# Performance work log

Hardware: AMD Instinct MI355X
Metric: run time of the kernel (lower is better)

## Reference

```python
import jax, jax.numpy as jnp
import numpy as np

D_MODEL = 768
D_FF = 3072
N_BEHAVIORS = 4
EPS = 1e-12


def layer_norm(x, g, b):
    m = jnp.mean(x, axis=-1, keepdims=True)
    v = jnp.mean(jnp.square(x - m), axis=-1, keepdims=True)
    return (x - m) * jax.lax.rsqrt(v + EPS) * g + b


def setup_inputs() -> dict:
    key = jax.random.key(0)
    ks = jax.random.split(key, 8)
    B, L = 8, 2048
    s1 = 1.0 / np.sqrt(D_MODEL)
    s2 = 1.0 / np.sqrt(D_FF)
    return {
        "input_tensor": jax.random.normal(ks[0], (B, L, D_MODEL), dtype=jnp.float32),
        "type_seq": jax.random.randint(ks[1], (B, L), 0, N_BEHAVIORS + 1),
        # per-behavior FeedForward params, stacked on leading n dim
        "W1": jax.random.normal(ks[2], (N_BEHAVIORS, D_MODEL, D_FF), dtype=jnp.float32) * s1,
        "b1": jnp.zeros((N_BEHAVIORS, D_FF), dtype=jnp.float32),
        "W2": jax.random.normal(ks[3], (N_BEHAVIORS, D_FF, D_MODEL), dtype=jnp.float32) * s2,
        "b2": jnp.zeros((N_BEHAVIORS, D_MODEL), dtype=jnp.float32),
        "ln_g": jnp.ones((N_BEHAVIORS, D_MODEL), dtype=jnp.float32),
        "ln_b": jnp.zeros((N_BEHAVIORS, D_MODEL), dtype=jnp.float32),
        # outer LayerNorm params
        "out_g": jnp.ones((D_MODEL,), dtype=jnp.float32),
        "out_b": jnp.zeros((D_MODEL,), dtype=jnp.float32),
    }


def reference(input_tensor, type_seq, W1, b1, W2, b2, ln_g, ln_b, out_g, out_b):
    n = W1.shape[0]
    # run every behavior's FeedForward over the full sequence (dense over-compute)
    h = jnp.einsum('BLH,nHF->nBLF', input_tensor, W1) + b1[:, None, None, :]
    h = jax.nn.gelu(h, approximate=False)  # torch 'gelu' = exact erf form
    h = jnp.einsum('nBLF,nFH->nBLH', h, W2) + b2[:, None, None, :]
    # per-expert residual LayerNorm (FeedForward with residual=True)
    h = layer_norm(h + input_tensor[None], ln_g[:, None, None, :], ln_b[:, None, None, :])
    # prepend zeros branch (class 0 = padding) then one-hot select per token
    stacked = jnp.concatenate([jnp.zeros_like(input_tensor)[None], h], axis=0)  # [n+1,B,L,H]
    onehot = jax.nn.one_hot(type_seq, n + 1, dtype=input_tensor.dtype)  # [B,L,n+1]
    sel = jnp.einsum('nBLH,BLn->BLH', stacked, onehot)
    # dropout is identity in eval; fused residual + LayerNorm
    return layer_norm(sel + input_tensor, out_g, out_b)
```

## Files before the change

kernel.cpp:

```cpp
#include <hip/hip_runtime.h>
#include <hip/hip_bf16.h>
#include <math.h>

#define NTOK   16384
#define DM     768
#define DF     3072
#define NEXP   4
#define TILE_SH (128 * 32)

#define XBLKS  6144
#define W1BLKS 2304
#define W2BLKS 2304
#define PREP_BLKS (1 + XBLKS + W1BLKS + W2BLKS)

typedef short bf16x8 __attribute__((ext_vector_type(8)));
typedef float f32x4  __attribute__((ext_vector_type(4)));

#define WS_CNT    0u
#define WS_BASES  256u
#define WS_POS    512u
#define WS_LIST   (512u + 65536u)
#define WS_XB     (WS_LIST + 262144u)
#define WS_W1T    (WS_XB + 25165824u)
#define WS_W2T    (WS_W1T + 18874368u)
#define WS_H1     (WS_W2T + 18874368u)
#define WS_H2     (WS_H1 + 100663296u)
#define WS_END    (WS_H2 + 25165824u)

__device__ __forceinline__ ushort f2bf(float f) {
    unsigned int v; __builtin_memcpy(&v, &f, 4);
    v = v + 0x7fffu + ((v >> 16) & 1u);
    return (ushort)(v >> 16);
}
__device__ __forceinline__ float bf2f(ushort u) {
    unsigned int v = ((unsigned int)u) << 16;
    float f; __builtin_memcpy(&f, &v, 4); return f;
}

__device__ __forceinline__ float fast_gelu(float v) {
    float y = v + 0.044715f * v * v * v;
    float e = __builtin_amdgcn_exp2f(-2.3022082f * y);
    return v * __builtin_amdgcn_rcpf(1.0f + e);
}

typedef __attribute__((address_space(1))) const void gvoid_t;
typedef __attribute__((address_space(3))) void lvoid_t;
__device__ __forceinline__ void cp16(const void* g, void* l) {
    __builtin_amdgcn_global_load_lds((gvoid_t*)g, (lvoid_t*)l, 16, 0, 0);
}

__device__ __forceinline__ int xcd_remap(int id, int T) {
    const int q = T >> 3, r = T & 7;
    const int x = id & 7, j = id >> 3;
    return (x < r ? x * (q + 1) : r * (q + 1) + (x - r) * q) + j;
}

__device__ __forceinline__ void transpose_tile(
    const float* __restrict__ src, ushort* __restrict__ dst, int R, int C,
    int bx, int by, int tid, ushort* tile ) {
    const int r0 = by * 64, c0 = bx * 64;
#pragma unroll
    for (int q = 0; q < 2; ++q) {
        int li = q * 256 + tid;
        int r = li >> 3, c = (li & 7) * 8;
        const float* s = src + (size_t)(r0 + r) * C + (c0 + c);
        float4 v0 = *(const float4*)s;
        float4 v1 = *(const float4*)(s + 4);
        ushort tmp[8];
        tmp[0] = f2bf(v0.x); tmp[1] = f2bf(v0.y); tmp[2] = f2bf(v0.z); tmp[3] = f2bf(v0.w);
        tmp[4] = f2bf(v1.x); tmp[5] = f2bf(v1.y); tmp[6] = f2bf(v1.z); tmp[7] = f2bf(v1.w);
        int sw = (((c >> 3) ^ ((r >> 3) & 7)) << 3);
        *(uint4*)&tile[r * 72 + sw] = *(uint4*)tmp;
    }
    __syncthreads();
#pragma unroll
    for (int q = 0; q < 2; ++q) {
        int li = q * 256 + tid;
        int r = li >> 3, c = (li & 7) * 8;
        ushort tmp[8];
#pragma unroll
        for (int j = 0; j < 8; ++j)
            tmp[j] = tile[(c + j) * 72 +
                          ((((r >> 3) & 7) ^ (((c + j) >> 3) & 7)) << 3) + (r & 7)];
        *(uint4*)(dst + (size_t)(c0 + r) * R + (r0 + c)) = *(uint4*)tmp;
    }
}

__global__ __launch_bounds__(256) void prep_kernel(
    const int* __restrict__ type_seq, const float* __restrict__ X,
    const float* __restrict__ W1, const float* __restrict__ W2,
    int* __restrict__ cnt, int* __restrict__ bases,
    int* __restrict__ pos_of, int* __restrict__ list,
    ushort* __restrict__ Xb, ushort* __restrict__ W1t, ushort* __restrict__ W2t) {
    __shared__ ushort tile[64 * 72];
    __shared__ int lcnt[NEXP];
    const int tid = threadIdx.x;
    const int bid = blockIdx.x;

    if (bid == 0) {
        if (tid < NEXP) lcnt[tid] = 0;
        __syncthreads();
        const int lane = tid & 63;
        for (int it = 0; it < NTOK / 256; ++it) {
            int t = it * 256 + tid;
            int k = type_seq[t];
#pragma unroll
            for (int e = 0; e < NEXP; ++e) {
                unsigned long long m = __ballot(k == e + 1);
                int total = __popcll(m);
                int b = 0;
                if (lane == 0 && total) b = atomicAdd(&lcnt[e], total);
                b = __shfl(b, 0, 64);
                if (k == e + 1) {
                    int p = b + __popcll(m & ((1ull << lane) - 1ull));
                    list[e * NTOK + p] = t;
                    pos_of[t] = p;
                }
            }
        }
        __syncthreads();
        if (tid == 0) {
            int s = 0, mb = 0;
            for (int e = 0; e < NEXP; ++e) {
                cnt[e] = lcnt[e];
                bases[e] = s;
                bases[8 + e] = mb;
                s += lcnt[e];
                mb += (lcnt[e] + 127) >> 7;
            }
            bases[12] = mb;
        }
        return;
    }

    int id = bid - 1;
    if (id < XBLKS) {
        size_t i = (size_t)(id * 256 + tid) * 8;
        float4 v0 = *(const float4*)(X + i);
        float4 v1 = *(const float4*)(X + i + 4);
        ushort tmp[8];
        tmp[0] = f2bf(v0.x); tmp[1] = f2bf(v0.y); tmp[2] = f2bf(v0.z); tmp[3] = f2bf(v0.w);
        tmp[4] = f2bf(v1.x); tmp[5] = f2bf(v1.y); tmp[6] = f2bf(v1.z); tmp[7] = f2bf(v1.w);
        *(uint4*)(Xb + i) = *(uint4*)tmp;
        return;
    }
    id -= XBLKS;
    if (id < W1BLKS) {
        int z = id / 576, r = id % 576;
        size_t mb = (size_t)z * DM * DF;
        transpose_tile(W1 + mb, W1t + mb, DM, DF, r % 48, r / 48, tid, tile);
        return;
    }
    id -= W1BLKS;
    {
        int z = id / 576, r = id % 576;
        size_t mb = (size_t)z * DF * DM;
        transpose_tile(W2 + mb, W2t + mb, DF, DM, r % 12, r / 12, tid, tile);
    }
}


__global__ __launch_bounds__(512, 4) void gemm1_kernel(
    const ushort* __restrict__ Xb, const ushort* __restrict__ W1t,
    const float* __restrict__ b1, const int* __restrict__ cnt,
    const int* __restrict__ bases, const int* __restrict__ list,
    ushort* __restrict__ h1) {
    const int mb = bases[12];
    const int T = mb * 24;
    int id = blockIdx.y * 24 + blockIdx.x;
    if (id >= T) return;
    id = xcd_remap(id, T);
    const int y = id / 24;
    const int n0 = (id % 24) * 128;
    const int* mboff = bases + 8;
    const int e = (y >= mboff[1]) + (y >= mboff[2]) + (y >= mboff[3]);
    const int m0 = (y - mboff[e]) << 7;
    const int count = cnt[e];
    const int NK = DM / 32;

    __shared__ __align__(16) short As[2 * TILE_SH];
    __shared__ __align__(16) short Bs[2 * TILE_SH];

    const int tid = threadIdx.x;
    const int wave = tid >> 6, lane = tid & 63;
    const int wm = (wave & 1) * 64, wn = (wave >> 1) * 32;
    const int lrow = lane & 15;
    const int qg = lane >> 4;

    int r0 = min(m0 + (tid >> 2), count - 1);
    int t0 = list[e * NTOK + r0];
    const int qsrc = ((tid & 3) ^ ((tid >> 3) & 3)) * 8;
    const ushort* a0 = Xb + (size_t)t0 * DM + qsrc;
    const ushort* Wb = W1t + (size_t)e * DF * DM;
    const ushort* bp0 = Wb + (size_t)(n0 + (tid >> 2)) * DM + qsrc;

    short* aDst = As + tid * 8;
    short* bDst = Bs + tid * 8;

    int aOff[4], bOff[2];
#pragma unroll
    for (int i = 0; i < 4; ++i) {
        int ra = wm + i * 16 + lrow;
        aOff[i] = ra * 32 + (qg ^ ((ra >> 1) & 3)) * 8;
    }
#pragma unroll
    for (int j = 0; j < 2; ++j) {
        int rb = wn + j * 16 + lrow;
        bOff[j] = rb * 32 + (qg ^ ((rb >> 1) & 3)) * 8;
    }

    f32x4 z = {0.f, 0.f, 0.f, 0.f};
    f32x4 acc[4][2];
#pragma unroll
    for (int i = 0; i < 4; ++i)
#pragma unroll
        for (int j = 0; j < 2; ++j) acc[i][j] = z;

    cp16(a0, aDst); cp16(bp0, bDst);
    a0 += 32; bp0 += 32;

    for (int ks = 0; ks < NK; ++ks) {
        __syncthreads();
        const int nsel = ((ks + 1) & 1) * TILE_SH;
        if (ks + 1 < NK) {
            cp16(a0, aDst + nsel); cp16(bp0, bDst + nsel);
            a0 += 32; bp0 += 32;
        }
        const short* Ab = As + (ks & 1) * TILE_SH;
        const short* Bb = Bs + (ks & 1) * TILE_SH;
        bf16x8 av[4], bv[2];
#pragma unroll
        for (int i = 0; i < 4; ++i) av[i] = *(const bf16x8*)(Ab + aOff[i]);
#pragma unroll
        for (int j = 0; j < 2; ++j) bv[j] = *(const bf16x8*)(Bb + bOff[j]);
#pragma unroll
        for (int i = 0; i < 4; ++i)
#pragma unroll
            for (int j = 0; j < 2; ++j)
                acc[i][j] = __builtin_amdgcn_mfma_f32_16x16x32_bf16(av[i], bv[j], acc[i][j], 0, 0, 0);
    }

    const int base = bases[e];
    float bias[2];
#pragma unroll
    for (int nt = 0; nt < 2; ++nt)
        bias[nt] = b1[e * DF + n0 + wn + nt * 16 + lrow];
#pragma unroll
    for (int mt = 0; mt < 4; ++mt) {
        int gm = m0 + wm + mt * 16 + (lane >> 4) * 4;
#pragma unroll
        for (int nt = 0; nt < 2; ++nt) {
            int gn = n0 + wn + nt * 16 + lrow;
#pragma unroll
            for (int r = 0; r < 4; ++r) {
                int i = gm + r;
                if (i < count) {
                    float v = acc[mt][nt][r] + bias[nt];
                    h1[(size_t)(base + i) * DF + gn] = f2bf(fast_gelu(v));
                }
            }
        }
    }
}

__global__ __launch_bounds__(512, 4) void gemm2_kernel(
    const ushort* __restrict__ h1, const ushort* __restrict__ W2t,
    const float* __restrict__ b2, const int* __restrict__ cnt,
    const int* __restrict__ bases, ushort* __restrict__ h2) {
    const int mb = bases[12];
    const int T = mb * 6;
    int id = blockIdx.y * 6 + blockIdx.x;
    if (id >= T) return;
    id = xcd_remap(id, T);
    const int y = id / 6;
    const int n0 = (id % 6) * 128;
    const int* mboff = bases + 8;
    const int e = (y >= mboff[1]) + (y >= mboff[2]) + (y >= mboff[3]);
    const int m0 = (y - mboff[e]) << 7;
    const int count = cnt[e];
    const int base = bases[e];
    const int NK = DF / 32;

    __shared__ __align__(16) short As[2 * TILE_SH];
    __shared__ __align__(16) short Bs[2 * TILE_SH];

    const int tid = threadIdx.x;
    const int wave = tid >> 6, lane = tid & 63;
    const int wm = (wave & 1) * 64, wn = (wave >> 1) * 32;
    const int lrow = lane & 15;
    const int qg = lane >> 4;

    int r0 = min(m0 + (tid >> 2), count - 1);
    const int qsrc = ((tid & 3) ^ ((tid >> 3) & 3)) * 8;
    const ushort* a0 = h1 + (size_t)(base + r0) * DF + qsrc;
    const ushort* Wb = W2t + (size_t)e * DM * DF;
    const ushort* bp0 = Wb + (size_t)(n0 + (tid >> 2)) * DF + qsrc;

    short* aDst = As + tid * 8;
    short* bDst = Bs + tid * 8;

    int aOff[4], bOff[2];
#pragma unroll
    for (int i = 0; i < 4; ++i) {
        int ra = wm + i * 16 + lrow;
        aOff[i] = ra * 32 + (qg ^ ((ra >> 1) & 3)) * 8;
    }
#pragma unroll
    for (int j = 0; j < 2; ++j) {
        int rb = wn + j * 16 + lrow;
        bOff[j] = rb * 32 + (qg ^ ((rb >> 1) & 3)) * 8;
    }

    f32x4 z = {0.f, 0.f, 0.f, 0.f};
    f32x4 acc[4][2];
#pragma unroll
    for (int i = 0; i < 4; ++i)
#pragma unroll
        for (int j = 0; j < 2; ++j) acc[i][j] = z;

    cp16(a0, aDst); cp16(bp0, bDst);
    a0 += 32; bp0 += 32;

    for (int ks = 0; ks < NK; ++ks) {
        __syncthreads();
        const int nsel = ((ks + 1) & 1) * TILE_SH;
        if (ks + 1 < NK) {
            cp16(a0, aDst + nsel); cp16(bp0, bDst + nsel);
            a0 += 32; bp0 += 32;
        }
        const short* Ab = As + (ks & 1) * TILE_SH;
        const short* Bb = Bs + (ks & 1) * TILE_SH;
        bf16x8 av[4], bv[2];
#pragma unroll
        for (int i = 0; i < 4; ++i) av[i] = *(const bf16x8*)(Ab + aOff[i]);
#pragma unroll
        for (int j = 0; j < 2; ++j) bv[j] = *(const bf16x8*)(Bb + bOff[j]);
#pragma unroll
        for (int i = 0; i < 4; ++i)
#pragma unroll
            for (int j = 0; j < 2; ++j)
                acc[i][j] = __builtin_amdgcn_mfma_f32_16x16x32_bf16(av[i], bv[j], acc[i][j], 0, 0, 0);
    }

    float bias[2];
#pragma unroll
    for (int nt = 0; nt < 2; ++nt)
        bias[nt] = b2[e * DM + n0 + wn + nt * 16 + lrow];
#pragma unroll
    for (int mt = 0; mt < 4; ++mt) {
        int gm = m0 + wm + mt * 16 + (lane >> 4) * 4;
#pragma unroll
        for (int nt = 0; nt < 2; ++nt) {
            int gn = n0 + wn + nt * 16 + lrow;
#pragma unroll
            for (int r = 0; r < 4; ++r) {
                int i = gm + r;
                if (i < count)
                    h2[(size_t)(base + i) * DM + gn] = f2bf(acc[mt][nt][r] + bias[nt]);
            }
        }
    }
}

__device__ __forceinline__ void block_reduce2(float& a, float& b, float* sm, int tid) {
    __syncthreads();
#pragma unroll
    for (int off = 32; off > 0; off >>= 1) {
        a += __shfl_down(a, off, 64);
        b += __shfl_down(b, off, 64);
    }
    const int wave = tid >> 6, lane = tid & 63;
    if (lane == 0) { sm[wave] = a; sm[4 + wave] = b; }
    __syncthreads();
    a = sm[0] + sm[1] + sm[2] + sm[3];
    b = sm[4] + sm[5] + sm[6] + sm[7];
}

__global__ __launch_bounds__(256) void finalize_kernel(
    const float* __restrict__ X, const int* __restrict__ type_seq,
    const int* __restrict__ pos_of, const int* __restrict__ bases,
    const ushort* __restrict__ h2,
    const float* __restrict__ ln_g, const float* __restrict__ ln_b,
    const float* __restrict__ out_g, const float* __restrict__ out_b,
    float* __restrict__ out) {
    __shared__ float sm[8];
    const int t = blockIdx.x;
    const int tid = threadIdx.x;
    const int k = type_seq[t];

    float xv[3], rv[3];
#pragma unroll
    for (int j = 0; j < 3; ++j) xv[j] = X[(size_t)t * DM + j * 256 + tid];

    if (k > 0) {
        const int e = k - 1;
        const size_t row = (size_t)(bases[e] + pos_of[t]);
        float v[3], s1 = 0.f, s2 = 0.f;
#pragma unroll
        for (int j = 0; j < 3; ++j) {
            v[j] = bf2f(h2[row * DM + j * 256 + tid]) + xv[j];
            s1 += v[j]; s2 += v[j] * v[j];
        }
        block_reduce2(s1, s2, sm, tid);
        float m = s1 * (1.f / DM);
        float inv = rsqrtf(s2 * (1.f / DM) - m * m + 1e-12f);
#pragma unroll
        for (int j = 0; j < 3; ++j) {
            int c = j * 256 + tid;
            rv[j] = (v[j] - m) * inv * ln_g[e * DM + c] + ln_b[e * DM + c];
        }
    } else {
        rv[0] = rv[1] = rv[2] = 0.f;
    }

    float w[3], s1 = 0.f, s2 = 0.f;
#pragma unroll
    for (int j = 0; j < 3; ++j) {
        w[j] = rv[j] + xv[j];
        s1 += w[j]; s2 += w[j] * w[j];
    }
    block_reduce2(s1, s2, sm, tid);
    float m = s1 * (1.f / DM);
    float inv = rsqrtf(s2 * (1.f / DM) - m * m + 1e-12f);
#pragma unroll
    for (int j = 0; j < 3; ++j) {
        int c = j * 256 + tid;
        out[(size_t)t * DM + c] = (w[j] - m) * inv * out_g[c] + out_b[c];
    }
}

extern "C" void kernel_launch(void* const* d_in, const int* in_sizes, int n_in,
                              void* d_out, int out_size, void* d_ws, size_t ws_size,
                              hipStream_t stream) {
    if (ws_size < (size_t)WS_END) return;

    const float* X     = (const float*)d_in[0];
    const int*   type  = (const int*)d_in[1];
    const float* W1    = (const float*)d_in[2];
    const float* b1    = (const float*)d_in[3];
    const float* W2    = (const float*)d_in[4];
    const float* b2    = (const float*)d_in[5];
    const float* ln_g  = (const float*)d_in[6];
    const float* ln_b  = (const float*)d_in[7];
    const float* out_g = (const float*)d_in[8];
    const float* out_b = (const float*)d_in[9];
    float* out = (float*)d_out;

    char* ws = (char*)d_ws;
    int* cnt    = (int*)(ws + WS_CNT);
    int* bases  = (int*)(ws + WS_BASES);
    int* pos_of = (int*)(ws + WS_POS);
    int* list   = (int*)(ws + WS_LIST);
    ushort* Xb  = (ushort*)(ws + WS_XB);
    ushort* W1t = (ushort*)(ws + WS_W1T);
    ushort* W2t = (ushort*)(ws + WS_W2T);
    ushort* h1  = (ushort*)(ws + WS_H1);
    ushort* h2  = (ushort*)(ws + WS_H2);

    prep_kernel<<<PREP_BLKS, 256, 0, stream>>>(type, X, W1, W2,
                                               cnt, bases, pos_of, list, Xb, W1t, W2t);
    gemm1_kernel<<<dim3(DF / 128, 132), 512, 0, stream>>>(Xb, W1t, b1, cnt, bases, list, h1);
    gemm2_kernel<<<dim3(DM / 128, 132), 512, 0, stream>>>(h1, W2t, b2, cnt, bases, h2);
    finalize_kernel<<<NTOK, 256, 0, stream>>>(X, type, pos_of, bases, h2, ln_g, ln_b, out_g, out_b, out);
}
```

Measured before the change: 427.8 us.

## Enlarge grouped GEMM tiles to 256x256 with BK=64 and deeper prefetch pipeline

Both expert GEMMs move from 128x128 tiles with K-step 32 to 256x256 tiles with K-step 64. Each wave now computes a 128x64 sub-tile. Loads are issued two stages ahead and guarded by explicit vmcnt waits and raw s_barrier, and MFMA priority is raised with setprio while the next stage is fetched. The larger tiles raise arithmetic intensity and cut barrier count per FLOP, at the cost of 128KB of LDS per block, fewer resident blocks, more padding waste on per-expert row tails, and a smaller grid that may leave CUs underused.

```diff
diff --git a/kernel.cpp b/kernel.cpp
--- a/kernel.cpp
+++ b/kernel.cpp
@@ -6,12 +6,13 @@
 #define DM     768
 #define DF     3072
 #define NEXP   4
-#define TILE_SH (128 * 32)
 
 #define XBLKS  6144
 #define W1BLKS 2304
 #define W2BLKS 2304
 #define PREP_BLKS (1 + XBLKS + W1BLKS + W2BLKS)
+
+#define MAXP   68
 
 typedef short bf16x8 __attribute__((ext_vector_type(8)));
 typedef float f32x4  __attribute__((ext_vector_type(4)));
@@ -126,7 +127,7 @@
                 bases[e] = s;
                 bases[8 + e] = mb;
                 s += lcnt[e];
-                mb += (lcnt[e] + 127) >> 7;
+                mb += (lcnt[e] + 255) >> 8;
             }
             bases[12] = mb;
         }
@@ -160,203 +161,250 @@
 }
 
 
-__global__ __launch_bounds__(512, 4) void gemm1_kernel(
+__global__ __launch_bounds__(512, 2) void gemm1_kernel(
     const ushort* __restrict__ Xb, const ushort* __restrict__ W1t,
     const float* __restrict__ b1, const int* __restrict__ cnt,
     const int* __restrict__ bases, const int* __restrict__ list,
     ushort* __restrict__ h1) {
     const int mb = bases[12];
-    const int T = mb * 24;
-    int id = blockIdx.y * 24 + blockIdx.x;
+    const int T = mb * 12;
+    int id = blockIdx.y * 12 + blockIdx.x;
     if (id >= T) return;
     id = xcd_remap(id, T);
-    const int y = id / 24;
-    const int n0 = (id % 24) * 128;
+    const int y = id / 12;
+    const int n0 = (id % 12) * 256;
     const int* mboff = bases + 8;
     const int e = (y >= mboff[1]) + (y >= mboff[2]) + (y >= mboff[3]);
-    const int m0 = (y - mboff[e]) << 7;
+    const int m0 = (y - mboff[e]) << 8;
     const int count = cnt[e];
-    const int NK = DM / 32;
-
-    __shared__ __align__(16) short As[2 * TILE_SH];
-    __shared__ __align__(16) short Bs[2 * TILE_SH];
+    const int base = bases[e];
+
+    __shared__ __align__(16) short As[2][16384];
+    __shared__ __align__(16) short Bs[2][16384];
 
     const int tid = threadIdx.x;
     const int wave = tid >> 6, lane = tid & 63;
-    const int wm = (wave & 1) * 64, wn = (wave >> 1) * 32;
-    const int lrow = lane & 15;
-    const int qg = lane >> 4;
-
-    int r0 = min(m0 + (tid >> 2), count - 1);
-    int t0 = list[e * NTOK + r0];
-    const int qsrc = ((tid & 3) ^ ((tid >> 3) & 3)) * 8;
-    const ushort* a0 = Xb + (size_t)t0 * DM + qsrc;
+    const int wr = wave >> 2, wc = wave & 3;
+    const int lrow = lane & 15, qg = lane >> 4;
+
+    const int rbase = tid >> 3;
+    const int qsrc = ((tid & 7) ^ (rbase & 7)) * 8;
+    const ushort* aP[4];
+#pragma unroll
+    for (int s = 0; s < 4; ++s) {
+        int r = min(m0 + rbase + s * 64, count - 1);
+        aP[s] = Xb + (size_t)list[e * NTOK + r] * DM + qsrc;
+    }
     const ushort* Wb = W1t + (size_t)e * DF * DM;
-    const ushort* bp0 = Wb + (size_t)(n0 + (tid >> 2)) * DM + qsrc;
-
-    short* aDst = As + tid * 8;
-    short* bDst = Bs + tid * 8;
-
-    int aOff[4], bOff[2];
-#pragma unroll
-    for (int i = 0; i < 4; ++i) {
-        int ra = wm + i * 16 + lrow;
-        aOff[i] = ra * 32 + (qg ^ ((ra >> 1) & 3)) * 8;
-    }
-#pragma unroll
-    for (int j = 0; j < 2; ++j) {
-        int rb = wn + j * 16 + lrow;
-        bOff[j] = rb * 32 + (qg ^ ((rb >> 1) & 3)) * 8;
-    }
-
-    f32x4 z = {0.f, 0.f, 0.f, 0.f};
-    f32x4 acc[4][2];
-#pragma unroll
-    for (int i = 0; i < 4; ++i)
-#pragma unroll
-        for (int j = 0; j < 2; ++j) acc[i][j] = z;
-
-    cp16(a0, aDst); cp16(bp0, bDst);
-    a0 += 32; bp0 += 32;
-
+    const ushort* bP = Wb + (size_t)(n0 + rbase) * DM + qsrc;
+
+    int aOff[8], bOff[4];
+#pragma unroll
+    for (int i = 0; i < 8; ++i) {
+        int r = wr * 128 + i * 16 + lrow;
+        aOff[i] = r * 64 + (qg ^ (lrow & 7)) * 8;
+    }
+#pragma unroll
+    for (int j = 0; j < 4; ++j) {
+        int r = wc * 64 + j * 16 + lrow;
+        bOff[j] = r * 64 + (qg ^ (lrow & 7)) * 8;
+    }
+
+    f32x4 acc[8][4];
+    f32x4 zz = {0.f, 0.f, 0.f, 0.f};
+#pragma unroll
+    for (int i = 0; i < 8; ++i)
+#pragma unroll
+        for (int j = 0; j < 4; ++j) acc[i][j] = zz;
+
+    auto STAGE = [&](int buf) {
+        short* aD = &As[buf][0] + tid * 8;
+        short* bD = &Bs[buf][0] + tid * 8;
+#pragma unroll
+        for (int s = 0; s < 4; ++s) { cp16(aP[s], aD + s * 4096); aP[s] += 64; }
+#pragma unroll
+        for (int s = 0; s < 4; ++s) cp16(bP + (size_t)s * 64 * DM, bD + s * 4096);
+        bP += 64;
+    };
+
+    STAGE(0); STAGE(1);
+    asm volatile("s_waitcnt vmcnt(8)" ::: "memory");
+    __builtin_amdgcn_s_barrier();
+
+    const int NK = DM / 64;
     for (int ks = 0; ks < NK; ++ks) {
-        __syncthreads();
-        const int nsel = ((ks + 1) & 1) * TILE_SH;
-        if (ks + 1 < NK) {
-            cp16(a0, aDst + nsel); cp16(bp0, bDst + nsel);
-            a0 += 32; bp0 += 32;
-        }
-        const short* Ab = As + (ks & 1) * TILE_SH;
-        const short* Bb = Bs + (ks & 1) * TILE_SH;
-        bf16x8 av[4], bv[2];
-#pragma unroll
-        for (int i = 0; i < 4; ++i) av[i] = *(const bf16x8*)(Ab + aOff[i]);
-#pragma unroll
-        for (int j = 0; j < 2; ++j) bv[j] = *(const bf16x8*)(Bb + bOff[j]);
-#pragma unroll
-        for (int i = 0; i < 4; ++i)
-#pragma unroll
-            for (int j = 0; j < 2; ++j)
-                acc[i][j] = __builtin_amdgcn_mfma_f32_16x16x32_bf16(av[i], bv[j], acc[i][j], 0, 0, 0);
-    }
-
-    const int base = bases[e];
-    float bias[2];
-#pragma unroll
-    for (int nt = 0; nt < 2; ++nt)
-        bias[nt] = b1[e * DF + n0 + wn + nt * 16 + lrow];
-#pragma unroll
-    for (int mt = 0; mt < 4; ++mt) {
-        int gm = m0 + wm + mt * 16 + (lane >> 4) * 4;
-#pragma unroll
-        for (int nt = 0; nt < 2; ++nt) {
-            int gn = n0 + wn + nt * 16 + lrow;
+        const short* Ab = &As[ks & 1][0];
+        const short* Bb = &Bs[ks & 1][0];
+        bf16x8 a0[8], b0[4];
+#pragma unroll
+        for (int i = 0; i < 8; ++i) a0[i] = *(const bf16x8*)(Ab + aOff[i]);
+#pragma unroll
+        for (int j = 0; j < 4; ++j) b0[j] = *(const bf16x8*)(Bb + bOff[j]);
+#pragma unroll
+        for (int i = 0; i < 8; ++i)
+#pragma unroll
+            for (int j = 0; j < 4; ++j)
+                acc[i][j] = __builtin_amdgcn_mfma_f32_16x16x32_bf16(a0[i], b0[j], acc[i][j], 0, 0, 0);
+        bf16x8 a1[8], b1v[4];
+#pragma unroll
+        for (int i = 0; i < 8; ++i) a1[i] = *(const bf16x8*)(Ab + (aOff[i] ^ 32));
+#pragma unroll
+        for (int j = 0; j < 4; ++j) b1v[j] = *(const bf16x8*)(Bb + (bOff[j] ^ 32));
+        asm volatile("s_waitcnt lgkmcnt(0)" ::: "memory");
+        __builtin_amdgcn_sched_barrier(0);
+        __builtin_amdgcn_s_barrier();
+        if (ks + 2 < NK) STAGE(ks & 1);
+        __builtin_amdgcn_s_setprio(1);
+#pragma unroll
+        for (int i = 0; i < 8; ++i)
+#pragma unroll
+            for (int j = 0; j < 4; ++j)
+                acc[i][j] = __builtin_amdgcn_mfma_f32_16x16x32_bf16(a1[i], b1v[j], acc[i][j], 0, 0, 0);
+        __builtin_amdgcn_s_setprio(0);
+        __builtin_amdgcn_sched_barrier(0);
+        if (ks + 2 < NK) { asm volatile("s_waitcnt vmcnt(8)" ::: "memory"); }
+        else             { asm volatile("s_waitcnt vmcnt(0)" ::: "memory"); }
+        __builtin_amdgcn_s_barrier();
+    }
+
+    float bias[4];
+#pragma unroll
+    for (int j = 0; j < 4; ++j) bias[j] = b1[e * DF + n0 + wc * 64 + j * 16 + lrow];
+#pragma unroll
+    for (int i = 0; i < 8; ++i) {
+        int gm = m0 + wr * 128 + i * 16 + qg * 4;
+#pragma unroll
+        for (int j = 0; j < 4; ++j) {
+            int gn = n0 + wc * 64 + j * 16 + lrow;
 #pragma unroll
             for (int r = 0; r < 4; ++r) {
-                int i = gm + r;
-                if (i < count) {
-                    float v = acc[mt][nt][r] + bias[nt];
-                    h1[(size_t)(base + i) * DF + gn] = f2bf(fast_gelu(v));
-                }
+                int row = gm + r;
+                if (row < count)
+                    h1[(size_t)(base + row) * DF + gn] = f2bf(fast_gelu(acc[i][j][r] + bias[j]));
             }
         }
     }
 }
 
-__global__ __launch_bounds__(512, 4) void gemm2_kernel(
+__global__ __launch_bounds__(512, 2) void gemm2_kernel(
     const ushort* __restrict__ h1, const ushort* __restrict__ W2t,
     const float* __restrict__ b2, const int* __restrict__ cnt,
     const int* __restrict__ bases, ushort* __restrict__ h2) {
     const int mb = bases[12];
-    const int T = mb * 6;
-    int id = blockIdx.y * 6 + blockIdx.x;
+    const int T = mb * 3;
+    int id = blockIdx.y * 3 + blockIdx.x;
     if (id >= T) return;
     id = xcd_remap(id, T);
-    const int y = id / 6;
-    const int n0 = (id % 6) * 128;
+    const int y = id / 3;
+    const int n0 = (id % 3) * 256;
     const int* mboff = bases + 8;
     const int e = (y >= mboff[1]) + (y >= mboff[2]) + (y >= mboff[3]);
-    const int m0 = (y - mboff[e]) << 7;
+    const int m0 = (y - mboff[e]) << 8;
     const int count = cnt[e];
     const int base = bases[e];
-    const int NK = DF / 32;
-
-    __shared__ __align__(16) short As[2 * TILE_SH];
-    __shared__ __align__(16) short Bs[2 * TILE_SH];
+
+    __shared__ __align__(16) short As[2][16384];
+    __shared__ __align__(16) short Bs[2][16384];
 
     const int tid = threadIdx.x;
     const int wave = tid >> 6, lane = tid & 63;
-    const int wm = (wave & 1) * 64, wn = (wave >> 1) * 32;
-    const int lrow = lane & 15;
-    const int qg = lane >> 4;
-
-    int r0 = min(m0 + (tid >> 2), count - 1);
-    const int qsrc = ((tid & 3) ^ ((tid >> 3) & 3)) * 8;
-    const ushort* a0 = h1 + (size_t)(base + r0) * DF + qsrc;
+    const int wr = wave >> 2, wc = wave & 3;
+    const int lrow = lane & 15, qg = lane >> 4;
+
+    const int rbase = tid >> 3;
+    const int qsrc = ((tid & 7) ^ (rbase & 7)) * 8;
+    const ushort* aP[4];
+#pragma unroll
+    for (int s = 0; s < 4; ++s) {
+        int r = min(m0 + rbase + s * 64, count - 1);
+        aP[s] = h1 + (size_t)(base + r) * DF + qsrc;
+    }
     const ushort* Wb = W2t + (size_t)e * DM * DF;
-    const ushort* bp0 = Wb + (size_t)(n0 + (tid >> 2)) * DF + qsrc;
-
-    short* aDst = As + tid * 8;
-    short* bDst = Bs + tid * 8;
-
-    int aOff[4], bOff[2];
-#pragma unroll
-    for (int i = 0; i < 4; ++i) {
-        int ra = wm + i * 16 + lrow;
-        aOff[i] = ra * 32 + (qg ^ ((ra >> 1) & 3)) * 8;
-    }
-#pragma unroll
-    for (int j = 0; j < 2; ++j) {
-        int rb = wn + j * 16 + lrow;
-        bOff[j] = rb * 32 + (qg ^ ((rb >> 1) & 3)) * 8;
-    }
-
-    f32x4 z = {0.f, 0.f, 0.f, 0.f};
-    f32x4 acc[4][2];
-#pragma unroll
-    for (int i = 0; i < 4; ++i)
-#pragma unroll
-        for (int j = 0; j < 2; ++j) acc[i][j] = z;
-
-    cp16(a0, aDst); cp16(bp0, bDst);
-    a0 += 32; bp0 += 32;
-
+    const ushort* bP = Wb + (size_t)(n0 + rbase) * DF + qsrc;
+
+    int aOff[8], bOff[4];
+#pragma unroll
+    for (int i = 0; i < 8; ++i) {
+        int r = wr * 128 + i * 16 + lrow;
+        aOff[i] = r * 64 + (qg ^ (lrow & 7)) * 8;
+    }
+#pragma unroll
+    for (int j = 0; j < 4; ++j) {
+        int r = wc * 64 + j * 16 + lrow;
+        bOff[j] = r * 64 + (qg ^ (lrow & 7)) * 8;
+    }
+
+    f32x4 acc[8][4];
+    f32x4 zz = {0.f, 0.f, 0.f, 0.f};
+#pragma unroll
+    for (int i = 0; i < 8; ++i)
+#pragma unroll
+        for (int j = 0; j < 4; ++j) acc[i][j] = zz;
+
+    auto STAGE = [&](int buf) {
+        short* aD = &As[buf][0] + tid * 8;
+        short* bD = &Bs[buf][0] + tid * 8;
+#pragma unroll
+        for (int s = 0; s < 4; ++s) { cp16(aP[s], aD + s * 4096); aP[s] += 64; }
+#pragma unroll
+        for (int s = 0; s < 4; ++s) cp16(bP + (size_t)s * 64 * DF, bD + s * 4096);
+        bP += 64;
+    };
+
+    STAGE(0); STAGE(1);
+    asm volatile("s_waitcnt vmcnt(8)" ::: "memory");
+    __builtin_amdgcn_s_barrier();
+
+    const int NK = DF / 64;
     for (int ks = 0; ks < NK; ++ks) {
-        __syncthreads();
-        const int nsel = ((ks + 1) & 1) * TILE_SH;
-        if (ks + 1 < NK) {
-            cp16(a0, aDst + nsel); cp16(bp0, bDst + nsel);
-            a0 += 32; bp0 += 32;
-        }
-        const short* Ab = As + (ks & 1) * TILE_SH;
-        const short* Bb = Bs + (ks & 1) * TILE_SH;
-        bf16x8 av[4], bv[2];
-#pragma unroll
-        for (int i = 0; i < 4; ++i) av[i] = *(const bf16x8*)(Ab + aOff[i]);
-#pragma unroll
-        for (int j = 0; j < 2; ++j) bv[j] = *(const bf16x8*)(Bb + bOff[j]);
-#pragma unroll
-        for (int i = 0; i < 4; ++i)
-#pragma unroll
-            for (int j = 0; j < 2; ++j)
-                acc[i][j] = __builtin_amdgcn_mfma_f32_16x16x32_bf16(av[i], bv[j], acc[i][j], 0, 0, 0);
-    }
-
-    float bias[2];
-#pragma unroll
-    for (int nt = 0; nt < 2; ++nt)
-        bias[nt] = b2[e * DM + n0 + wn + nt * 16 + lrow];
-#pragma unroll
-    for (int mt = 0; mt < 4; ++mt) {
-        int gm = m0 + wm + mt * 16 + (lane >> 4) * 4;
-#pragma unroll
-        for (int nt = 0; nt < 2; ++nt) {
-            int gn = n0 + wn + nt * 16 + lrow;
+        const short* Ab = &As[ks & 1][0];
+        const short* Bb = &Bs[ks & 1][0];
+        bf16x8 a0[8], b0[4];
+#pragma unroll
+        for (int i = 0; i < 8; ++i) a0[i] = *(const bf16x8*)(Ab + aOff[i]);
+#pragma unroll
+        for (int j = 0; j < 4; ++j) b0[j] = *(const bf16x8*)(Bb + bOff[j]);
+#pragma unroll
+        for (int i = 0; i < 8; ++i)
+#pragma unroll
+            for (int j = 0; j < 4; ++j)
+                acc[i][j] = __builtin_amdgcn_mfma_f32_16x16x32_bf16(a0[i], b0[j], acc[i][j], 0, 0, 0);
+        bf16x8 a1[8], b1v[4];
+#pragma unroll
+        for (int i = 0; i < 8; ++i) a1[i] = *(const bf16x8*)(Ab + (aOff[i] ^ 32));
+#pragma unroll
+        for (int j = 0; j < 4; ++j) b1v[j] = *(const bf16x8*)(Bb + (bOff[j] ^ 32));
+        asm volatile("s_waitcnt lgkmcnt(0)" ::: "memory");
+        __builtin_amdgcn_sched_barrier(0);
+        __builtin_amdgcn_s_barrier();
+        if (ks + 2 < NK) STAGE(ks & 1);
+        __builtin_amdgcn_s_setprio(1);
+#pragma unroll
+        for (int i = 0; i < 8; ++i)
+#pragma unroll
+            for (int j = 0; j < 4; ++j)
+                acc[i][j] = __builtin_amdgcn_mfma_f32_16x16x32_bf16(a1[i], b1v[j], acc[i][j], 0, 0, 0);
+        __builtin_amdgcn_s_setprio(0);
+        __builtin_amdgcn_sched_barrier(0);
+        if (ks + 2 < NK) { asm volatile("s_waitcnt vmcnt(8)" ::: "memory"); }
+        else             { asm volatile("s_waitcnt vmcnt(0)" ::: "memory"); }
+        __builtin_amdgcn_s_barrier();
+    }
+
+    float bias[4];
+#pragma unroll
+    for (int j = 0; j < 4; ++j) bias[j] = b2[e * DM + n0 + wc * 64 + j * 16 + lrow];
+#pragma unroll
+    for (int i = 0; i < 8; ++i) {
+        int gm = m0 + wr * 128 + i * 16 + qg * 4;
+#pragma unroll
+        for (int j = 0; j < 4; ++j) {
+            int gn = n0 + wc * 64 + j * 16 + lrow;
 #pragma unroll
             for (int r = 0; r < 4; ++r) {
-                int i = gm + r;
-                if (i < count)
-                    h2[(size_t)(base + i) * DM + gn] = f2bf(acc[mt][nt][r] + bias[nt]);
+                int row = gm + r;
+                if (row < count)
+                    h2[(size_t)(base + row) * DM + gn] = f2bf(acc[i][j][r] + bias[j]);
             }
         }
     }
@@ -459,7 +507,7 @@
 
     prep_kernel<<<PREP_BLKS, 256, 0, stream>>>(type, X, W1, W2,
                                                cnt, bases, pos_of, list, Xb, W1t, W2t);
-    gemm1_kernel<<<dim3(DF / 128, 132), 512, 0, stream>>>(Xb, W1t, b1, cnt, bases, list, h1);
-    gemm2_kernel<<<dim3(DM / 128, 132), 512, 0, stream>>>(h1, W2t, b2, cnt, bases, h2);
+    gemm1_kernel<<<dim3(12, MAXP), 512, 0, stream>>>(Xb, W1t, b1, cnt, bases, list, h1);
+    gemm2_kernel<<<dim3(3, MAXP), 512, 0, stream>>>(h1, W2t, b2, cnt, bases, h2);
     finalize_kernel<<<NTOK, 256, 0, stream>>>(X, type, pos_of, bases, h2, ln_g, ln_b, out_g, out_b, out);
 }
```

Measured after the change: 464.2 us. 8.5% more time.

## Use 4-wave blocks with 64x64 per-wave tiles in both expert GEMMs

Applied to the files above, without the earlier changes.

Both grouped GEMM kernels go from 512-thread blocks (8 waves, 64x32 each) to 256-thread blocks (4 waves, 64x64 each), keeping the 128x128 block tile. Each wave now reuses 4 A fragments across 4 B fragments (16 MFMAs per 8 LDS reads instead of 8 per 6), and each thread issues two async loads per operand per stage. The LDS swizzle index is also rewritten to follow the row. The cost is more accumulator registers per thread (64 floats) and fewer waves to hide latency, which could lower occupancy.

```diff
diff --git a/kernel.cpp b/kernel.cpp
--- a/kernel.cpp
+++ b/kernel.cpp
@@ -6,12 +6,13 @@
 #define DM     768
 #define DF     3072
 #define NEXP   4
-#define TILE_SH (128 * 32)
 
 #define XBLKS  6144
 #define W1BLKS 2304
 #define W2BLKS 2304
 #define PREP_BLKS (1 + XBLKS + W1BLKS + W2BLKS)
+
+#define MAXP   132
 
 typedef short bf16x8 __attribute__((ext_vector_type(8)));
 typedef float f32x4  __attribute__((ext_vector_type(4)));
@@ -160,7 +161,7 @@
 }
 
 
-__global__ __launch_bounds__(512, 4) void gemm1_kernel(
+__global__ __launch_bounds__(256) void gemm1_kernel(
     const ushort* __restrict__ Xb, const ushort* __restrict__ W1t,
     const float* __restrict__ b1, const int* __restrict__ cnt,
     const int* __restrict__ bases, const int* __restrict__ list,
@@ -176,94 +177,91 @@
     const int e = (y >= mboff[1]) + (y >= mboff[2]) + (y >= mboff[3]);
     const int m0 = (y - mboff[e]) << 7;
     const int count = cnt[e];
+    const int base = bases[e];
     const int NK = DM / 32;
 
-    __shared__ __align__(16) short As[2 * TILE_SH];
-    __shared__ __align__(16) short Bs[2 * TILE_SH];
+    __shared__ __align__(16) short As[2][4096];
+    __shared__ __align__(16) short Bs[2][4096];
 
     const int tid = threadIdx.x;
     const int wave = tid >> 6, lane = tid & 63;
-    const int wm = (wave & 1) * 64, wn = (wave >> 1) * 32;
-    const int lrow = lane & 15;
-    const int qg = lane >> 4;
-
-    int r0 = min(m0 + (tid >> 2), count - 1);
-    int t0 = list[e * NTOK + r0];
-    const int qsrc = ((tid & 3) ^ ((tid >> 3) & 3)) * 8;
-    const ushort* a0 = Xb + (size_t)t0 * DM + qsrc;
+    const int wm = (wave & 1) * 64, wn = (wave >> 1) * 64;
+    const int lrow = lane & 15, qg = lane >> 4;
+
+    const int rbase = tid >> 2;
+    const int qsrc = ((tid & 3) ^ ((rbase >> 1) & 3)) * 8;
+    int r0 = min(m0 + rbase, count - 1);
+    int r1 = min(m0 + rbase + 64, count - 1);
+    const ushort* aP0 = Xb + (size_t)list[e * NTOK + r0] * DM + qsrc;
+    const ushort* aP1 = Xb + (size_t)list[e * NTOK + r1] * DM + qsrc;
     const ushort* Wb = W1t + (size_t)e * DF * DM;
-    const ushort* bp0 = Wb + (size_t)(n0 + (tid >> 2)) * DM + qsrc;
-
-    short* aDst = As + tid * 8;
-    short* bDst = Bs + tid * 8;
-
-    int aOff[4], bOff[2];
+    const ushort* bP0 = Wb + (size_t)(n0 + rbase) * DM + qsrc;
+    const ushort* bP1 = bP0 + (size_t)64 * DM;
+
+    int aOff[4], bOff[4];
 #pragma unroll
     for (int i = 0; i < 4; ++i) {
         int ra = wm + i * 16 + lrow;
         aOff[i] = ra * 32 + (qg ^ ((ra >> 1) & 3)) * 8;
-    }
-#pragma unroll
-    for (int j = 0; j < 2; ++j) {
-        int rb = wn + j * 16 + lrow;
-        bOff[j] = rb * 32 + (qg ^ ((rb >> 1) & 3)) * 8;
-    }
-
-    f32x4 z = {0.f, 0.f, 0.f, 0.f};
-    f32x4 acc[4][2];
+        int rb = wn + i * 16 + lrow;
+        bOff[i] = rb * 32 + (qg ^ ((rb >> 1) & 3)) * 8;
+    }
+
+    f32x4 zz = {0.f, 0.f, 0.f, 0.f};
+    f32x4 acc[4][4];
 #pragma unroll
     for (int i = 0; i < 4; ++i)
 #pragma unroll
-        for (int j = 0; j < 2; ++j) acc[i][j] = z;
-
-    cp16(a0, aDst); cp16(bp0, bDst);
-    a0 += 32; bp0 += 32;
+        for (int j = 0; j < 4; ++j) acc[i][j] = zz;
+
+    auto STAGE = [&](int buf) {
+        short* aD = &As[buf][0] + tid * 8;
+        short* bD = &Bs[buf][0] + tid * 8;
+        cp16(aP0, aD); cp16(aP1, aD + 2048);
+        cp16(bP0, bD); cp16(bP1, bD + 2048);
+        aP0 += 32; aP1 += 32; bP0 += 32; bP1 += 32;
+    };
+
+    STAGE(0);
 
     for (int ks = 0; ks < NK; ++ks) {
         __syncthreads();
-        const int nsel = ((ks + 1) & 1) * TILE_SH;
-        if (ks + 1 < NK) {
-            cp16(a0, aDst + nsel); cp16(bp0, bDst + nsel);
-            a0 += 32; bp0 += 32;
-        }
-        const short* Ab = As + (ks & 1) * TILE_SH;
-        const short* Bb = Bs + (ks & 1) * TILE_SH;
-        bf16x8 av[4], bv[2];
+        if (ks + 1 < NK) STAGE((ks + 1) & 1);
+        const short* Ab = &As[ks & 1][0];
+        const short* Bb = &Bs[ks & 1][0];
+        bf16x8 av[4], bv[4];
 #pragma unroll
         for (int i = 0; i < 4; ++i) av[i] = *(const bf16x8*)(Ab + aOff[i]);
 #pragma unroll
-        for (int j = 0; j < 2; ++j) bv[j] = *(const bf16x8*)(Bb + bOff[j]);
+        for (int j = 0; j < 4; ++j) bv[j] = *(const bf16x8*)(Bb + bOff[j]);
 #pragma unroll
         for (int i = 0; i < 4; ++i)
 #pragma unroll
-            for (int j = 0; j < 2; ++j)
+            for (int j = 0; j < 4; ++j)
                 acc[i][j] = __builtin_amdgcn_mfma_f32_16x16x32_bf16(av[i], bv[j], acc[i][j], 0, 0, 0);
     }
 
-    const int base = bases[e];
-    float bias[2];
-#pragma unroll
-    for (int nt = 0; nt < 2; ++nt)
-        bias[nt] = b1[e * DF + n0 + wn + nt * 16 + lrow];
-#pragma unroll
-    for (int mt = 0; mt < 4; ++mt) {
-        int gm = m0 + wm + mt * 16 + (lane >> 4) * 4;
-#pragma unroll
-        for (int nt = 0; nt < 2; ++nt) {
-            int gn = n0 + wn + nt * 16 + lrow;
+    float bias[4];
+#pragma unroll
+    for (int j = 0; j < 4; ++j)
+        bias[j] = b1[e * DF + n0 + wn + j * 16 + lrow];
+#pragma unroll
+    for (int i = 0; i < 4; ++i) {
+        int gm = m0 + wm + i * 16 + qg * 4;
+#pragma unroll
+        for (int j = 0; j < 4; ++j) {
+            int gn = n0 + wn + j * 16 + lrow;
 #pragma unroll
             for (int r = 0; r < 4; ++r) {
-                int i = gm + r;
-                if (i < count) {
-                    float v = acc[mt][nt][r] + bias[nt];
-                    h1[(size_t)(base + i) * DF + gn] = f2bf(fast_gelu(v));
-                }
+                int row = gm + r;
+                if (row < count)
+                    h1[(size_t)(base + row) * DF + gn] = f2bf(fast_gelu(acc[i][j][r] + bias[j]));
             }
         }
     }
 }
 
-__global__ __launch_bounds__(512, 4) void gemm2_kernel(
+__global__ __launch_bounds__(256) void gemm2_kernel(
     const ushort* __restrict__ h1, const ushort* __restrict__ W2t,
     const float* __restrict__ b2, const int* __restrict__ cnt,
     const int* __restrict__ bases, ushort* __restrict__ h2) {
@@ -281,82 +279,82 @@
     const int base = bases[e];
     const int NK = DF / 32;
 
-    __shared__ __align__(16) short As[2 * TILE_SH];
-    __shared__ __align__(16) short Bs[2 * TILE_SH];
+    __shared__ __align__(16) short As[2][4096];
+    __shared__ __align__(16) short Bs[2][4096];
 
     const int tid = threadIdx.x;
     const int wave = tid >> 6, lane = tid & 63;
-    const int wm = (wave & 1) * 64, wn = (wave >> 1) * 32;
-    const int lrow = lane & 15;
-    const int qg = lane >> 4;
-
-    int r0 = min(m0 + (tid >> 2), count - 1);
-    const int qsrc = ((tid & 3) ^ ((tid >> 3) & 3)) * 8;
-    const ushort* a0 = h1 + (size_t)(base + r0) * DF + qsrc;
+    const int wm = (wave & 1) * 64, wn = (wave >> 1) * 64;
+    const int lrow = lane & 15, qg = lane >> 4;
+
+    const int rbase = tid >> 2;
+    const int qsrc = ((tid & 3) ^ ((rbase >> 1) & 3)) * 8;
+    int r0 = min(m0 + rbase, count - 1);
+    int r1 = min(m0 + rbase + 64, count - 1);
+    const ushort* aP0 = h1 + (size_t)(base + r0) * DF + qsrc;
+    const ushort* aP1 = h1 + (size_t)(base + r1) * DF + qsrc;
     const ushort* Wb = W2t + (size_t)e * DM * DF;
-    const ushort* bp0 = Wb + (size_t)(n0 + (tid >> 2)) * DF + qsrc;
-
-    short* aDst = As + tid * 8;
-    short* bDst = Bs + tid * 8;
-
-    int aOff[4], bOff[2];
+    const ushort* bP0 = Wb + (size_t)(n0 + rbase) * DF + qsrc;
+    const ushort* bP1 = bP0 + (size_t)64 * DF;
+
+    int aOff[4], bOff[4];
 #pragma unroll
     for (int i = 0; i < 4; ++i) {
         int ra = wm + i * 16 + lrow;
         aOff[i] = ra * 32 + (qg ^ ((ra >> 1) & 3)) * 8;
-    }
-#pragma unroll
-    for (int j = 0; j < 2; ++j) {
-        int rb = wn + j * 16 + lrow;
-        bOff[j] = rb * 32 + (qg ^ ((rb >> 1) & 3)) * 8;
-    }
-
-    f32x4 z = {0.f, 0.f, 0.f, 0.f};
-    f32x4 acc[4][2];
+        int rb = wn + i * 16 + lrow;
+        bOff[i] = rb * 32 + (qg ^ ((rb >> 1) & 3)) * 8;
+    }
+
+    f32x4 zz = {0.f, 0.f, 0.f, 0.f};
+    f32x4 acc[4][4];
 #pragma unroll
     for (int i = 0; i < 4; ++i)
 #pragma unroll
-        for (int j = 0; j < 2; ++j) acc[i][j] = z;
-
-    cp16(a0, aDst); cp16(bp0, bDst);
-    a0 += 32; bp0 += 32;
+        for (int j = 0; j < 4; ++j) acc[i][j] = zz;
+
+    auto STAGE = [&](int buf) {
+        short* aD = &As[buf][0] + tid * 8;
+        short* bD = &Bs[buf][0] + tid * 8;
+        cp16(aP0, aD); cp16(aP1, aD + 2048);
+        cp16(bP0, bD); cp16(bP1, bD + 2048);
+        aP0 += 32; aP1 += 32; bP0 += 32; bP1 += 32;
+    };
+
+    STAGE(0);
 
     for (int ks = 0; ks < NK; ++ks) {
         __syncthreads();
-        const int nsel = ((ks + 1) & 1) * TILE_SH;
-        if (ks + 1 < NK) {
-            cp16(a0, aDst + nsel); cp16(bp0, bDst + nsel);
-            a0 += 32; bp0 += 32;
-        }
-        const short* Ab = As + (ks & 1) * TILE_SH;
-        const short* Bb = Bs + (ks & 1) * TILE_SH;
-        bf16x8 av[4], bv[2];
+        if (ks + 1 < NK) STAGE((ks + 1) & 1);
+        const short* Ab = &As[ks & 1][0];
+        const short* Bb = &Bs[ks & 1][0];
+        bf16x8 av[4], bv[4];
 #pragma unroll
         for (int i = 0; i < 4; ++i) av[i] = *(const bf16x8*)(Ab + aOff[i]);
 #pragma unroll
-        for (int j = 0; j < 2; ++j) bv[j] = *(const bf16x8*)(Bb + bOff[j]);
+        for (int j = 0; j < 4; ++j) bv[j] = *(const bf16x8*)(Bb + bOff[j]);
 #pragma unroll
         for (int i = 0; i < 4; ++i)
 #pragma unroll
-            for (int j = 0; j < 2; ++j)
+            for (int j = 0; j < 4; ++j)
                 acc[i][j] = __builtin_amdgcn_mfma_f32_16x16x32_bf16(av[i], bv[j], acc[i][j], 0, 0, 0);
     }
 
-    float bias[2];
-#pragma unroll
-    for (int nt = 0; nt < 2; ++nt)
-        bias[nt] = b2[e * DM + n0 + wn + nt * 16 + lrow];
-#pragma unroll
-    for (int mt = 0; mt < 4; ++mt) {
-        int gm = m0 + wm + mt * 16 + (lane >> 4) * 4;
-#pragma unroll
-        for (int nt = 0; nt < 2; ++nt) {
-            int gn = n0 + wn + nt * 16 + lrow;
+    float bias[4];
+#pragma unroll
+    for (int j = 0; j < 4; ++j)
+        bias[j] = b2[e * DM + n0 + wn + j * 16 + lrow];
+#pragma unroll
+    for (int i = 0; i < 4; ++i) {
+        int gm = m0 + wm + i * 16 + qg * 4;
+#pragma unroll
+        for (int j = 0; j < 4; ++j) {
+            int gn = n0 + wn + j * 16 + lrow;
 #pragma unroll
             for (int r = 0; r < 4; ++r) {
-                int i = gm + r;
-                if (i < count)
-                    h2[(size_t)(base + i) * DM + gn] = f2bf(acc[mt][nt][r] + bias[nt]);
+                int row = gm + r;
+                if (row < count)
+                    h2[(size_t)(base + row) * DM + gn] = f2bf(acc[i][j][r] + bias[j]);
             }
         }
     }
@@ -459,7 +457,7 @@
 
     prep_kernel<<<PREP_BLKS, 256, 0, stream>>>(type, X, W1, W2,
                                                cnt, bases, pos_of, list, Xb, W1t, W2t);
-    gemm1_kernel<<<dim3(DF / 128, 132), 512, 0, stream>>>(Xb, W1t, b1, cnt, bases, list, h1);
-    gemm2_kernel<<<dim3(DM / 128, 132), 512, 0, stream>>>(h1, W2t, b2, cnt, bases, h2);
+    gemm1_kernel<<<dim3(24, MAXP), 256, 0, stream>>>(Xb, W1t, b1, cnt, bases, list, h1);
+    gemm2_kernel<<<dim3(6, MAXP), 256, 0, stream>>>(h1, W2t, b2, cnt, bases, h2);
     finalize_kernel<<<NTOK, 256, 0, stream>>>(X, type, pos_of, bases, h2, ln_g, ln_b, out_g, out_b, out);
 }
```

Result: slower. 462.0 us (+8.0%).
